# Kernel tuning notes

Hardware: AMD Instinct MI355X
Metric: run time of the kernel (lower is better)

## Reference

```python
import jax, jax.numpy as jnp
import numpy as np

MAX_SX = 10  # max_shiftx
MAX_SY = 10  # max_shifty
STD_EPS = 1e-9


def setup_inputs() -> dict:
    key = jax.random.key(0)
    x = jax.random.normal(key, (8, 32, 128, 128), dtype=jnp.float32)
    return {"x": x}


def _cross_correlation(x):
    b, c, h, w = x.shape
    n = h * w
    # _standartize: zero-mean, divide by (unbiased std * sqrt(h*w)); std<eps -> inf -> 0
    xc = x - jnp.mean(x, axis=(2, 3), keepdims=True)
    std = jnp.std(xc, axis=(2, 3), keepdims=True, ddof=1)
    std = jnp.where(std < STD_EPS, jnp.inf, std)
    xs = xc / (std * jnp.sqrt(jnp.asarray(n, x.dtype)))
    # FFT-based circular cross-correlation for all ordered pairs (i, j>=i)
    Xf = jnp.fft.fft2(xs)  # [b, c, h, w] complex
    ii, jj = np.triu_indices(c)  # row-major: (0,0),(0,1),...,(0,c-1),(1,1),... matches the loop order
    cross = Xf[:, ii] * jnp.conj(Xf[:, jj])  # [b, P, h, w], P = c*(c+1)//2
    cc = jnp.real(jnp.fft.ifft2(cross))
    # The [[br, bl], [tr, tl]] corner concat == roll by (sy, sx) then take leading window
    cc = jnp.roll(cc, (MAX_SY, MAX_SX), axis=(2, 3))
    return cc[:, :, : 2 * MAX_SY + 1, : 2 * MAX_SX + 1]  # [b, P, 2sy+1, 2sx+1]


def reference(x):
    return _cross_correlation(x)
```

## Files before the change

kernel.cpp:

```cpp
#include <hip/hip_runtime.h>
#include <hip/hip_bf16.h>

typedef __attribute__((ext_vector_type(4))) unsigned int uint4v;
typedef __attribute__((ext_vector_type(8))) short short8;
typedef __attribute__((ext_vector_type(16))) float floatx16;

#define NROW 148
#define ROWB (20*512)
#define BB   ((size_t)NROW*ROWB)
#define STATS_OFF ((size_t)8*BB)
#define LDS_A_ROWS 38
#define ABUF (LDS_A_ROWS*2048)
#define LDS_BYTES (2*ABUF)

__device__ __forceinline__ unsigned short f2b(float f){
  unsigned int u = __float_as_uint(f);
  return (unsigned short)((u + 0x7fffu + ((u >> 16) & 1u)) >> 16);
}

#define BAR_LGKM() do { \
  __builtin_amdgcn_sched_barrier(0); \
  asm volatile("s_waitcnt lgkmcnt(0)" ::: "memory"); \
  __builtin_amdgcn_s_barrier(); \
  __builtin_amdgcn_sched_barrier(0); \
} while(0)

__global__ __launch_bounds__(256) void k_stat(const float* __restrict__ x,
                                              float* __restrict__ stats){
  int bid = blockIdx.x;
  int t = threadIdx.x;
  const float* xc = x + ((size_t)bid << 14);
  float s = 0.f, ss = 0.f;
  #pragma unroll 4
  for (int k = 0; k < 64; ++k){
    float v = xc[t + (k << 8)];
    s += v; ss += v*v;
  }
  #pragma unroll
  for (int m = 32; m >= 1; m >>= 1){
    s  += __shfl_xor(s, m);
    ss += __shfl_xor(ss, m);
  }
  __shared__ float rs[4], rss[4];
  int wv = t >> 6, l = t & 63;
  if (l == 0){ rs[wv] = s; rss[wv] = ss; }
  __syncthreads();
  if (t == 0){
    float S  = rs[0]+rs[1]+rs[2]+rs[3];
    float SS = rss[0]+rss[1]+rss[2]+rss[3];
    float mean = S * (1.f/16384.f);
    float var  = (SS - S*mean) * (1.f/16383.f);
    float sd = sqrtf(fmaxf(var, 0.f));
    stats[bid*2]   = mean;
    stats[bid*2+1] = (sd < 1e-9f) ? 0.f : 1.f/(sd*128.f);
  }
}

__global__ __launch_bounds__(512) void k_pack(const float* __restrict__ x,
                                              const float* __restrict__ stats,
                                              unsigned char* __restrict__ pad){
  __shared__ float rowbuf[32*129];
  int bid = blockIdx.x;
  int b = bid & 7, rg = bid >> 3;
  int t = threadIdx.x;
  int ch = t >> 4, xq = t & 15;
  float mean  = stats[(b*32 + ch)*2];
  float scale = stats[(b*32 + ch)*2 + 1];
  const float* xc = x + ((size_t)(b*32 + ch) << 14);
  for (int rr = 0; rr < 4; ++rr){
    int r = rg*4 + rr;
    int sy = (r + 118) & 127;
    const float* src = xc + (sy << 7) + (xq << 3);
    float4 v0 = *(const float4*)src;
    float4 v1 = *(const float4*)(src + 4);
    float* rb = rowbuf + ch*129 + (xq << 3);
    rb[0] = (v0.x-mean)*scale; rb[1] = (v0.y-mean)*scale;
    rb[2] = (v0.z-mean)*scale; rb[3] = (v0.w-mean)*scale;
    rb[4] = (v1.x-mean)*scale; rb[5] = (v1.y-mean)*scale;
    rb[6] = (v1.z-mean)*scale; rb[7] = (v1.w-mean)*scale;
    __syncthreads();
    #pragma unroll
    for (int k = 0; k < 2; ++k){
      int q = t + (k << 9);
      if (q < 640){
        int col = q >> 5, cq = q & 31;
        const float* rbq = rowbuf + cq*129;
        unsigned int d[4];
        #pragma unroll
        for (int e = 0; e < 4; ++e){
          unsigned int lo = f2b(rbq[(8*col + 2*e)     & 127]);
          unsigned int hi = f2b(rbq[(8*col + 2*e + 1) & 127]);
          d[e] = lo | (hi << 16);
        }
        uint4v ov = {d[0], d[1], d[2], d[3]};
        *(uint4v*)(pad + ((size_t)(b*148 + r)*20 + col)*512 + cq*16) = ov;
      }
    }
    __syncthreads();
  }
}

#define WW(k3, idx) (aw[k3][(idx)>>2][(idx)&3])
#define SHIFT_STORE(OFS, ODD) \
  { _Pragma("unroll") \
    for (int k3 = 0; k3 < 3; ++k3){ \
      int pid = tid + (k3 << 9); \
      if (pid < 1216){ \
        char* dst = Asw + (pid >> 5)*2048 + (pid & 31)*16; \
        _Pragma("unroll") \
        for (int c = 0; c < 4; ++c){ \
          unsigned int o0,o1,o2,o3; \
          if (ODD){ \
            o0 = (WW(k3,4*c+OFS+0)>>16)|(WW(k3,4*c+OFS+1)<<16); \
            o1 = (WW(k3,4*c+OFS+1)>>16)|(WW(k3,4*c+OFS+2)<<16); \
            o2 = (WW(k3,4*c+OFS+2)>>16)|(WW(k3,4*c+OFS+3)<<16); \
            o3 = (WW(k3,4*c+OFS+3)>>16)|(WW(k3,4*c+OFS+4)<<16); \
          } else { \
            o0 = WW(k3,4*c+OFS+0); o1 = WW(k3,4*c+OFS+1); \
            o2 = WW(k3,4*c+OFS+2); o3 = WW(k3,4*c+OFS+3); \
          } \
          uint4v ov = {o0,o1,o2,o3}; \
          *(uint4v*)(dst + c*512) = ov; \
        } \
      } \
    } }
#define DO_SHIFT_STORE() \
  switch (r2){ \
    case 0: SHIFT_STORE(0, 0); break; \
    case 1: SHIFT_STORE(0, 1); break; \
    case 2: SHIFT_STORE(1, 0); break; \
    case 3: SHIFT_STORE(1, 1); break; \
    case 4: SHIFT_STORE(2, 0); break; \
    case 5: SHIFT_STORE(2, 1); break; \
    case 6: SHIFT_STORE(3, 0); break; \
    case 7: SHIFT_STORE(3, 1); break; \
  }

__global__ __launch_bounds__(512, 1) void k_corr(const unsigned char* __restrict__ pad,
                                                 float* __restrict__ out){
  extern __shared__ char lds[];
  char* As = lds;
  float* sf = (float*)lds;

  int bid = blockIdx.x;
  int b = bid & 7, cg = bid >> 3;
  int dx, d0;
  if (cg < 2){ dx = 0; d0 = cg << 2; }
  else { int q = cg - 2; dx = 1 + q/3; d0 = -10 + 7*(q - 3*(q/3)); }
  int r2 = dx & 7, cwoff = dx >> 3;

  int tid = threadIdx.x;
  int lane = tid & 63, wvi = tid >> 6;
  int ks = wvi & 1, kq = wvi >> 1;
  unsigned offF = (unsigned)((2*ks + (lane >> 5))*512 + (lane & 31)*16);

  const unsigned char* pb = pad + (size_t)b*BB;

  floatx16 acc[7];
  #pragma unroll
  for (int d = 0; d < 7; ++d) acc[d] = (floatx16)(0.0f);

  uint4v aw[3][5];
  auto issueA = [&](int tt){
    int rab = 32*(tt >> 2) + 10 + d0;
    int cwb = 4*(tt & 3) + cwoff;
    #pragma unroll
    for (int k3 = 0; k3 < 3; ++k3){
      int pid = tid + (k3 << 9);
      if (pid < 1216){
        const unsigned char* g = pb + ((size_t)((rab + (pid >> 5))*20 + cwb))*512 + (pid & 31)*16;
        #pragma unroll
        for (int kk = 0; kk < 5; ++kk)
          aw[k3][kk] = *(const uint4v*)(g + kk*512);
      }
    }
  };
  auto pBaddr = [&](int tt)->const unsigned char*{
    return pb + ((size_t)((32*(tt >> 2) + 10 + kq*8)*20 + 4*(tt & 3) + 2*ks))*512
              + (unsigned)((lane >> 5)*512 + (lane & 31)*16);
  };

  issueA(0);
  { char* Asw = As; DO_SHIFT_STORE(); }
  issueA(1);
  short8 BQ[4];
  {
    const unsigned char* pB0 = pBaddr(0);
    #pragma unroll
    for (int k = 0; k < 4; ++k) BQ[k] = *(const short8*)(pB0 + (size_t)k*ROWB);
  }
  BAR_LGKM();

  for (int t = 0; t < 16; ++t){
    if (t < 15){ char* Asw = As + ((t+1)&1)*ABUF; DO_SHIFT_STORE(); }
    if (t < 14) issueA(t+2);
    const char* Ab = As + (t&1)*ABUF + (kq*8)*2048 + offF;
    const unsigned char* pBc = pBaddr(t);
    const unsigned char* pBn = pBaddr(t+1);
    bool more = (t < 15);
    short8 ring[8];
    #pragma unroll
    for (int w = 0; w < 8; ++w) ring[w] = *(const short8*)(Ab + w*2048);
    __builtin_amdgcn_s_setprio(1);
    #pragma unroll
    for (int yl = 0; yl < 8; ++yl){
      short8 bf = BQ[yl & 3];
      #pragma unroll
      for (int d = 0; d < 7; ++d)
        acc[d] = __builtin_amdgcn_mfma_f32_32x32x16_bf16(ring[(yl+d)&7], bf, acc[d], 0, 0, 0);
      if (yl < 4)       BQ[yl & 3] = *(const short8*)(pBc + (size_t)(yl + 4)*ROWB);
      else if (more)    BQ[yl & 3] = *(const short8*)(pBn + (size_t)(yl - 4)*ROWB);
      if (yl < 6) ring[yl & 7] = *(const short8*)(Ab + (yl + 8)*2048);
    }
    __builtin_amdgcn_s_setprio(0);
    BAR_LGKM();
  }

  int baseb = b * 232848;
  #pragma unroll
  for (int d = 0; d < 7; ++d){
    #pragma unroll
    for (int r = 0; r < 16; ++r)
      sf[wvi*1024 + r*64 + lane] = acc[d][r];
    __syncthreads();
    int dy = d0 + d;
    #pragma unroll
    for (int k = 0; k < 2; ++k){
      int p = tid + (k << 9);
      float v = 0.f;
      #pragma unroll
      for (int w = 0; w < 8; ++w) v += sf[w*1024 + p];
      int reg = p >> 6, ln = p & 63;
      int i = (reg & 3) + 8*(reg >> 2) + 4*(ln >> 5);
      int j = ln & 31;
      if (i <= j){
        int pp = i*(65 - i)/2 + (j - i);
        out[baseb + pp*441 + (10+dy)*21 + (10+dx)] = v;
        if (i == j && (dy != 0 || dx != 0))
          out[baseb + pp*441 + (10-dy)*21 + (10-dx)] = v;
      } else {
        int pp = j*(65 - j)/2 + (i - j);
        out[baseb + pp*441 + (10-dy)*21 + (10-dx)] = v;
      }
    }
    __syncthreads();
  }
}

extern "C" void kernel_launch(void* const* d_in, const int* in_sizes, int n_in,
                              void* d_out, int out_size, void* d_ws, size_t ws_size,
                              hipStream_t stream){
  const float* x = (const float*)d_in[0];
  unsigned char* pad = (unsigned char*)d_ws;
  float* stats = (float*)((char*)d_ws + STATS_OFF);
  float* out = (float*)d_out;
  hipFuncSetAttribute((const void*)k_corr, hipFuncAttributeMaxDynamicSharedMemorySize,
                      LDS_BYTES);
  k_stat<<<dim3(256), dim3(256), 0, stream>>>(x, stats);
  k_pack<<<dim3(296), dim3(512), 0, stream>>>(x, stats, pad);
  k_corr<<<dim3(256), dim3(512), LDS_BYTES, stream>>>(pad, out);
}
```

Before: 81.11 us.

## Split correlation work across twice as many smaller blocks with separate reduction kernel

Each correlation block is halved to 256 threads and covers half the column range, so 512 blocks launch, up to two per CU, using a smaller single LDS buffer instead of double buffering. Partial sums are written to workspace, and a new reduction kernel adds the two halves and scatters them into the output. This aims to raise occupancy and CU utilisation on a GPU with more CUs than the old 256 blocks. The cost is lost double buffering (extra barriers per iteration), extra global traffic for the partials, and one more kernel launch.

```diff
diff --git a/kernel.cpp b/kernel.cpp
--- a/kernel.cpp
+++ b/kernel.cpp
@@ -9,9 +9,8 @@
 #define ROWB (20*512)
 #define BB   ((size_t)NROW*ROWB)
 #define STATS_OFF ((size_t)8*BB)
-#define LDS_A_ROWS 38
-#define ABUF (LDS_A_ROWS*2048)
-#define LDS_BYTES (2*ABUF)
+#define PART_OFF (STATS_OFF + 2048)
+#define LDS_A_ROWS 22
 
 __device__ __forceinline__ unsigned short f2b(float f){
   unsigned int u = __float_as_uint(f);
@@ -104,9 +103,9 @@
 #define SHIFT_STORE(OFS, ODD) \
   { _Pragma("unroll") \
     for (int k3 = 0; k3 < 3; ++k3){ \
-      int pid = tid + (k3 << 9); \
-      if (pid < 1216){ \
-        char* dst = Asw + (pid >> 5)*2048 + (pid & 31)*16; \
+      int pid = tid + (k3 << 8); \
+      if (pid < 704){ \
+        char* dst = As + (pid >> 5)*2048 + (pid & 31)*16; \
         _Pragma("unroll") \
         for (int c = 0; c < 4; ++c){ \
           unsigned int o0,o1,o2,o3; \
@@ -136,14 +135,12 @@
     case 7: SHIFT_STORE(3, 1); break; \
   }
 
-__global__ __launch_bounds__(512, 1) void k_corr(const unsigned char* __restrict__ pad,
-                                                 float* __restrict__ out){
-  extern __shared__ char lds[];
-  char* As = lds;
-  float* sf = (float*)lds;
-
-  int bid = blockIdx.x;
-  int b = bid & 7, cg = bid >> 3;
+__global__ __launch_bounds__(256, 2) void k_corr(const unsigned char* __restrict__ pad,
+                                                 float* __restrict__ part){
+  __shared__ alignas(16) char As[LDS_A_ROWS*2048];
+
+  int bid = blockIdx.x;
+  int b = bid & 7, xh = (bid >> 3) & 1, cg = bid >> 4;
   int dx, d0;
   if (cg < 2){ dx = 0; d0 = cg << 2; }
   else { int q = cg - 2; dx = 1 + q/3; d0 = -10 + 7*(q - 3*(q/3)); }
@@ -162,12 +159,12 @@
 
   uint4v aw[3][5];
   auto issueA = [&](int tt){
-    int rab = 32*(tt >> 2) + 10 + d0;
-    int cwb = 4*(tt & 3) + cwoff;
+    int rab = 16*(tt & 7) + 10 + d0;
+    int cwb = 4*(2*xh + (tt >> 3)) + cwoff;
     #pragma unroll
     for (int k3 = 0; k3 < 3; ++k3){
-      int pid = tid + (k3 << 9);
-      if (pid < 1216){
+      int pid = tid + (k3 << 8);
+      if (pid < 704){
         const unsigned char* g = pb + ((size_t)((rab + (pid >> 5))*20 + cwb))*512 + (pid & 31)*16;
         #pragma unroll
         for (int kk = 0; kk < 5; ++kk)
@@ -176,25 +173,26 @@
     }
   };
   auto pBaddr = [&](int tt)->const unsigned char*{
-    return pb + ((size_t)((32*(tt >> 2) + 10 + kq*8)*20 + 4*(tt & 3) + 2*ks))*512
+    int rbb = 16*(tt & 7) + 10 + kq*8;
+    int col = 4*(2*xh + (tt >> 3)) + 2*ks;
+    return pb + ((size_t)(rbb*20 + col))*512
               + (unsigned)((lane >> 5)*512 + (lane & 31)*16);
   };
 
   issueA(0);
-  { char* Asw = As; DO_SHIFT_STORE(); }
-  issueA(1);
   short8 BQ[4];
   {
     const unsigned char* pB0 = pBaddr(0);
     #pragma unroll
     for (int k = 0; k < 4; ++k) BQ[k] = *(const short8*)(pB0 + (size_t)k*ROWB);
   }
-  BAR_LGKM();
 
   for (int t = 0; t < 16; ++t){
-    if (t < 15){ char* Asw = As + ((t+1)&1)*ABUF; DO_SHIFT_STORE(); }
-    if (t < 14) issueA(t+2);
-    const char* Ab = As + (t&1)*ABUF + (kq*8)*2048 + offF;
+    BAR_LGKM();
+    DO_SHIFT_STORE();
+    BAR_LGKM();
+    if (t < 15) issueA(t+1);
+    const char* Ab = As + (kq*8)*2048 + offF;
     const unsigned char* pBc = pBaddr(t);
     const unsigned char* pBn = pBaddr(t+1);
     bool more = (t < 15);
@@ -213,23 +211,44 @@
       if (yl < 6) ring[yl & 7] = *(const short8*)(Ab + (yl + 8)*2048);
     }
     __builtin_amdgcn_s_setprio(0);
-    BAR_LGKM();
-  }
-
-  int baseb = b * 232848;
+  }
+
+  BAR_LGKM();
+  float* sf = (float*)As;
+  size_t pbase = (size_t)bid * 7168;
   #pragma unroll
   for (int d = 0; d < 7; ++d){
     #pragma unroll
     for (int r = 0; r < 16; ++r)
       sf[wvi*1024 + r*64 + lane] = acc[d][r];
     __syncthreads();
+    #pragma unroll
+    for (int k = 0; k < 4; ++k){
+      int p = tid + (k << 8);
+      part[pbase + d*1024 + p] = sf[p] + sf[1024 + p] + sf[2048 + p] + sf[3072 + p];
+    }
+    __syncthreads();
+  }
+}
+
+__global__ __launch_bounds__(256) void k_red(const float* __restrict__ part,
+                                             float* __restrict__ out){
+  int bid = blockIdx.x;
+  int b = bid & 7, cg = bid >> 3;
+  int dx, d0;
+  if (cg < 2){ dx = 0; d0 = cg << 2; }
+  else { int q = cg - 2; dx = 1 + q/3; d0 = -10 + 7*(q - 3*(q/3)); }
+  const float* pA = part + (size_t)(cg*16 + b)*7168;
+  const float* pB = part + (size_t)(cg*16 + 8 + b)*7168;
+  int t = threadIdx.x;
+  int baseb = b * 232848;
+  #pragma unroll
+  for (int d = 0; d < 7; ++d){
     int dy = d0 + d;
     #pragma unroll
-    for (int k = 0; k < 2; ++k){
-      int p = tid + (k << 9);
-      float v = 0.f;
-      #pragma unroll
-      for (int w = 0; w < 8; ++w) v += sf[w*1024 + p];
+    for (int k = 0; k < 4; ++k){
+      int p = t + (k << 8);
+      float v = pA[d*1024 + p] + pB[d*1024 + p];
       int reg = p >> 6, ln = p & 63;
       int i = (reg & 3) + 8*(reg >> 2) + 4*(ln >> 5);
       int j = ln & 31;
@@ -243,7 +262,6 @@
         out[baseb + pp*441 + (10-dy)*21 + (10-dx)] = v;
       }
     }
-    __syncthreads();
   }
 }
 
@@ -253,10 +271,10 @@
   const float* x = (const float*)d_in[0];
   unsigned char* pad = (unsigned char*)d_ws;
   float* stats = (float*)((char*)d_ws + STATS_OFF);
+  float* part  = (float*)((char*)d_ws + PART_OFF);
   float* out = (float*)d_out;
-  hipFuncSetAttribute((const void*)k_corr, hipFuncAttributeMaxDynamicSharedMemorySize,
-                      LDS_BYTES);
   k_stat<<<dim3(256), dim3(256), 0, stream>>>(x, stats);
   k_pack<<<dim3(296), dim3(512), 0, stream>>>(x, stats, pad);
-  k_corr<<<dim3(256), dim3(512), LDS_BYTES, stream>>>(pad, out);
-}
+  k_corr<<<dim3(512), dim3(256), 0, stream>>>(pad, part);
+  k_red <<<dim3(256), dim3(256), 0, stream>>>(part, out);
+}
```

Result: slower. 94.26 us (+16.2%).

## Stage shifted A tiles via direct global-to-LDS loads using pre-shifted packed copies

Applied to the files above, without the earlier changes.

The pack kernel now writes two bf16 copies of the padded input, one shifted by a single column, so odd horizontal shifts no longer need register-level 16-bit realignment. The correlation kernel drops the register staging and shift-and-store step and uses 4-byte global_load_lds instructions to fill the double-buffered LDS A tile directly. This removes VGPR pressure and VALU work from the main loop, but doubles the packed workspace written by k_pack and issues many small 4-byte DMA loads instead of 16-byte vector loads. Barriers become plain __syncthreads.

```diff
diff --git a/kernel.cpp b/kernel.cpp
--- a/kernel.cpp
+++ b/kernel.cpp
@@ -8,7 +8,8 @@
 #define NROW 148
 #define ROWB (20*512)
 #define BB   ((size_t)NROW*ROWB)
-#define STATS_OFF ((size_t)8*BB)
+#define COPYB ((size_t)8*BB)
+#define STATS_OFF ((size_t)2*COPYB)
 #define LDS_A_ROWS 38
 #define ABUF (LDS_A_ROWS*2048)
 #define LDS_BYTES (2*ABUF)
@@ -18,12 +19,10 @@
   return (unsigned short)((u + 0x7fffu + ((u >> 16) & 1u)) >> 16);
 }
 
-#define BAR_LGKM() do { \
-  __builtin_amdgcn_sched_barrier(0); \
-  asm volatile("s_waitcnt lgkmcnt(0)" ::: "memory"); \
-  __builtin_amdgcn_s_barrier(); \
-  __builtin_amdgcn_sched_barrier(0); \
-} while(0)
+__device__ __forceinline__ void gload_lds4(const void* g, void* l){
+  __builtin_amdgcn_global_load_lds((const __attribute__((address_space(1))) unsigned int*)g,
+                                   (__attribute__((address_space(3))) unsigned int*)l, 4, 0, 0);
+}
 
 __global__ __launch_bounds__(256) void k_stat(const float* __restrict__ x,
                                               float* __restrict__ stats){
@@ -80,66 +79,32 @@
     rb[6] = (v1.z-mean)*scale; rb[7] = (v1.w-mean)*scale;
     __syncthreads();
     #pragma unroll
-    for (int k = 0; k < 2; ++k){
+    for (int k = 0; k < 3; ++k){
       int q = t + (k << 9);
-      if (q < 640){
-        int col = q >> 5, cq = q & 31;
+      if (q < 1280){
+        int p = (q >= 640) ? 1 : 0;
+        int qq = q - p*640;
+        int col = qq >> 5, cq = qq & 31;
         const float* rbq = rowbuf + cq*129;
         unsigned int d[4];
         #pragma unroll
         for (int e = 0; e < 4; ++e){
-          unsigned int lo = f2b(rbq[(8*col + 2*e)     & 127]);
-          unsigned int hi = f2b(rbq[(8*col + 2*e + 1) & 127]);
+          unsigned int lo = f2b(rbq[(8*col + 2*e + p)     & 127]);
+          unsigned int hi = f2b(rbq[(8*col + 2*e + 1 + p) & 127]);
           d[e] = lo | (hi << 16);
         }
         uint4v ov = {d[0], d[1], d[2], d[3]};
-        *(uint4v*)(pad + ((size_t)(b*148 + r)*20 + col)*512 + cq*16) = ov;
+        *(uint4v*)(pad + (size_t)p*COPYB
+                   + ((size_t)(b*148 + r)*20 + col)*512 + cq*16) = ov;
       }
     }
     __syncthreads();
   }
 }
-
-#define WW(k3, idx) (aw[k3][(idx)>>2][(idx)&3])
-#define SHIFT_STORE(OFS, ODD) \
-  { _Pragma("unroll") \
-    for (int k3 = 0; k3 < 3; ++k3){ \
-      int pid = tid + (k3 << 9); \
-      if (pid < 1216){ \
-        char* dst = Asw + (pid >> 5)*2048 + (pid & 31)*16; \
-        _Pragma("unroll") \
-        for (int c = 0; c < 4; ++c){ \
-          unsigned int o0,o1,o2,o3; \
-          if (ODD){ \
-            o0 = (WW(k3,4*c+OFS+0)>>16)|(WW(k3,4*c+OFS+1)<<16); \
-            o1 = (WW(k3,4*c+OFS+1)>>16)|(WW(k3,4*c+OFS+2)<<16); \
-            o2 = (WW(k3,4*c+OFS+2)>>16)|(WW(k3,4*c+OFS+3)<<16); \
-            o3 = (WW(k3,4*c+OFS+3)>>16)|(WW(k3,4*c+OFS+4)<<16); \
-          } else { \
-            o0 = WW(k3,4*c+OFS+0); o1 = WW(k3,4*c+OFS+1); \
-            o2 = WW(k3,4*c+OFS+2); o3 = WW(k3,4*c+OFS+3); \
-          } \
-          uint4v ov = {o0,o1,o2,o3}; \
-          *(uint4v*)(dst + c*512) = ov; \
-        } \
-      } \
-    } }
-#define DO_SHIFT_STORE() \
-  switch (r2){ \
-    case 0: SHIFT_STORE(0, 0); break; \
-    case 1: SHIFT_STORE(0, 1); break; \
-    case 2: SHIFT_STORE(1, 0); break; \
-    case 3: SHIFT_STORE(1, 1); break; \
-    case 4: SHIFT_STORE(2, 0); break; \
-    case 5: SHIFT_STORE(2, 1); break; \
-    case 6: SHIFT_STORE(3, 0); break; \
-    case 7: SHIFT_STORE(3, 1); break; \
-  }
 
 __global__ __launch_bounds__(512, 1) void k_corr(const unsigned char* __restrict__ pad,
                                                  float* __restrict__ out){
   extern __shared__ char lds[];
-  char* As = lds;
   float* sf = (float*)lds;
 
   int bid = blockIdx.x;
@@ -147,32 +112,34 @@
   int dx, d0;
   if (cg < 2){ dx = 0; d0 = cg << 2; }
   else { int q = cg - 2; dx = 1 + q/3; d0 = -10 + 7*(q - 3*(q/3)); }
-  int r2 = dx & 7, cwoff = dx >> 3;
+  int p = dx & 1, dxe = dx - p;
 
   int tid = threadIdx.x;
   int lane = tid & 63, wvi = tid >> 6;
   int ks = wvi & 1, kq = wvi >> 1;
   unsigned offF = (unsigned)((2*ks + (lane >> 5))*512 + (lane & 31)*16);
 
-  const unsigned char* pb = pad + (size_t)b*BB;
+  const unsigned char* pb  = pad + (size_t)b*BB;
+  const unsigned char* pbp = pad + (size_t)p*COPYB + (size_t)b*BB;
+
+  int tmp = dxe + 2*(lane & 3);
+  unsigned phi = (unsigned)(((tmp >> 3) << 9) + ((lane >> 2) << 4) + ((tmp & 6) << 1));
 
   floatx16 acc[7];
   #pragma unroll
   for (int d = 0; d < 7; ++d) acc[d] = (floatx16)(0.0f);
 
-  uint4v aw[3][5];
-  auto issueA = [&](int tt){
+  auto stageA = [&](int tt, char* dstbuf){
     int rab = 32*(tt >> 2) + 10 + d0;
-    int cwb = 4*(tt & 3) + cwoff;
-    #pragma unroll
-    for (int k3 = 0; k3 < 3; ++k3){
-      int pid = tid + (k3 << 9);
-      if (pid < 1216){
-        const unsigned char* g = pb + ((size_t)((rab + (pid >> 5))*20 + cwb))*512 + (pid & 31)*16;
-        #pragma unroll
-        for (int kk = 0; kk < 5; ++kk)
-          aw[k3][kk] = *(const uint4v*)(g + kk*512);
-      }
+    int xi4 = (tt & 3) << 2;
+    int u0 = wvi * 38;
+    #pragma unroll
+    for (int s = 0; s < 38; ++s){
+      int u = u0 + s;
+      int r = u >> 3, i = u & 7;
+      const unsigned char* g = pbp + (size_t)(rab + r)*ROWB
+            + (unsigned)(((xi4 + (i >> 1)) << 9) + ((i & 1) << 8)) + phi;
+      gload_lds4(g, dstbuf + (unsigned)u*256);
     }
   };
   auto pBaddr = [&](int tt)->const unsigned char*{
@@ -180,21 +147,18 @@
               + (unsigned)((lane >> 5)*512 + (lane & 31)*16);
   };
 
-  issueA(0);
-  { char* Asw = As; DO_SHIFT_STORE(); }
-  issueA(1);
+  stageA(0, lds);
   short8 BQ[4];
   {
     const unsigned char* pB0 = pBaddr(0);
     #pragma unroll
     for (int k = 0; k < 4; ++k) BQ[k] = *(const short8*)(pB0 + (size_t)k*ROWB);
   }
-  BAR_LGKM();
+  __syncthreads();
 
   for (int t = 0; t < 16; ++t){
-    if (t < 15){ char* Asw = As + ((t+1)&1)*ABUF; DO_SHIFT_STORE(); }
-    if (t < 14) issueA(t+2);
-    const char* Ab = As + (t&1)*ABUF + (kq*8)*2048 + offF;
+    if (t < 15) stageA(t+1, lds + ((t+1)&1)*ABUF);
+    const char* Ab = lds + (t&1)*ABUF + (kq*8)*2048 + offF;
     const unsigned char* pBc = pBaddr(t);
     const unsigned char* pBn = pBaddr(t+1);
     bool more = (t < 15);
@@ -213,7 +177,7 @@
       if (yl < 6) ring[yl & 7] = *(const short8*)(Ab + (yl + 8)*2048);
     }
     __builtin_amdgcn_s_setprio(0);
-    BAR_LGKM();
+    __syncthreads();
   }
 
   int baseb = b * 232848;
@@ -226,11 +190,11 @@
     int dy = d0 + d;
     #pragma unroll
     for (int k = 0; k < 2; ++k){
-      int p = tid + (k << 9);
+      int pp0 = tid + (k << 9);
       float v = 0.f;
       #pragma unroll
-      for (int w = 0; w < 8; ++w) v += sf[w*1024 + p];
-      int reg = p >> 6, ln = p & 63;
+      for (int w = 0; w < 8; ++w) v += sf[w*1024 + pp0];
+      int reg = pp0 >> 6, ln = pp0 & 63;
       int i = (reg & 3) + 8*(reg >> 2) + 4*(ln >> 5);
       int j = ln & 31;
       if (i <= j){
```

Result: slower. 139.1 us (+71.5%).
